# Performance work log

Hardware: AMD Instinct MI355X
Metric: run time of the kernel (lower is better)

## Reference

```python
import jax, jax.numpy as jnp
import numpy as np

N = 100_000      # nodes
E = 1_600_000    # edges (avg degree 16)
D_IN = 128
H = 512


def setup_inputs() -> dict:
    key = jax.random.key(0)
    ks = jax.random.split(key, 7)
    x = jax.random.normal(ks[0], (N, D_IN), dtype=jnp.float32)
    edge_index = jax.random.randint(ks[1], (2, E), 0, N, dtype=jnp.int32)
    s_in = 1.0 / np.sqrt(D_IN).astype(np.float32)
    s_h = 1.0 / np.sqrt(H).astype(np.float32)
    # SAGEConv params: lin_l applied to aggregated neighbors (has bias), lin_r to root
    W_l = jax.random.uniform(ks[2], (D_IN, H), jnp.float32, -s_in, s_in)
    b_l = jax.random.uniform(ks[3], (H,), jnp.float32, -s_in, s_in)
    W_r = jax.random.uniform(ks[4], (D_IN, H), jnp.float32, -s_in, s_in)
    # final projection Linear(hidden, hidden)
    W_proj = jax.random.uniform(ks[5], (H, H), jnp.float32, -s_h, s_h)
    b_proj = jax.random.uniform(ks[6], (H,), jnp.float32, -s_h, s_h)
    return {"x": x, "edge_index": edge_index, "W_l": W_l, "b_l": b_l,
            "W_r": W_r, "W_proj": W_proj, "b_proj": b_proj}


def reference(x, edge_index, W_l, b_l, W_r, W_proj, b_proj):
    src, dst = edge_index[0], edge_index[1]
    # mean aggregation of neighbor features: gather x[src], scatter-add to dst
    agg = jax.ops.segment_sum(x[src], dst, num_segments=N)          # [N, D_IN]
    deg = jax.ops.segment_sum(jnp.ones((E,), x.dtype), dst, num_segments=N)
    mean = agg / jnp.maximum(deg, 1.0)[:, None]
    # SAGEConv: lin_l(mean_neighbors) + lin_r(x)
    h = mean @ W_l + b_l + x @ W_r                                   # [N, H]
    h = jax.nn.relu(h)                                               # dropout: eval mode (identity)
    return h @ W_proj + b_proj                                       # [N, H]
```

## Files before the change

### kernel.cpp

```cpp
#include <hip/hip_runtime.h>
#include <hip/hip_bf16.h>

#define DIN  128
#define HID  512
#define K1   256
#define NPAD 96
#define BSH  8
#define CAPSH 13
#define EPB  4096

typedef __attribute__((ext_vector_type(8))) short short8;
typedef __attribute__((ext_vector_type(4))) float f32x4;

__device__ inline ushort bf16rne(float f) {
    union { float f; unsigned u; } c; c.f = f;
    unsigned b = c.u + 0x7fff + ((c.u >> 16) & 1);
    return (ushort)(b >> 16);
}
__device__ inline float bf16tof(unsigned lo16) {
    union { unsigned u; float f; } c; c.u = lo16 << 16;
    return c.f;
}
__device__ __forceinline__ void gld16(const void* g, void* l) {
    __builtin_amdgcn_global_load_lds((const __attribute__((address_space(1))) unsigned int*)g,
                                     (__attribute__((address_space(3))) unsigned int*)l, 16, 0, 0);
}

__global__ void prep_w(const float* __restrict__ Wl, const float* __restrict__ Wr,
                       const float* __restrict__ Wp,
                       ushort* __restrict__ W1L, ushort* __restrict__ W2L) {
    int t = blockIdx.x * blockDim.x + threadIdx.x;
    if (t < 8 * 4 * 512) {
        int p = t >> 11, c = (t >> 9) & 3, col = t & 511;
        int k0 = p * 32 + c * 8;
        #pragma unroll
        for (int r = 0; r < 8; ++r) {
            int k = k0 + r;
            float v = (k < DIN) ? Wl[k * HID + col] : Wr[(k - DIN) * HID + col];
            W1L[(size_t)t * 8 + r] = bf16rne(v);
        }
    } else if (t < 8 * 4 * 512 + 16 * 4 * 512) {
        int t2 = t - 8 * 4 * 512;
        int p = t2 >> 11, c = (t2 >> 9) & 3, col = t2 & 511;
        int k0 = p * 32 + c * 8;
        #pragma unroll
        for (int r = 0; r < 8; ++r)
            W2L[(size_t)t2 * 8 + r] = bf16rne(Wp[(k0 + r) * HID + col]);
    }
}

__global__ void xcvt(const float* __restrict__ x, ushort* __restrict__ xb, int total4) {
    int i = blockIdx.x * blockDim.x + threadIdx.x;
    if (i >= total4) return;
    const float4 v = ((const float4*)x)[i];
    ushort4 o;
    o.x = bf16rne(v.x); o.y = bf16rne(v.y); o.z = bf16rne(v.z); o.w = bf16rne(v.w);
    ((ushort4*)xb)[i] = o;
}

__global__ void binit_kernel(int* __restrict__ bcur, int nb) {
    int i = threadIdx.x + blockIdx.x * 1024;
    if (i < nb) bcur[i] = i << CAPSH;
}

__global__ __launch_bounds__(256) void bucket_kernel(
    const int* __restrict__ ei, int* __restrict__ bcur,
    unsigned* __restrict__ eb, int E, int nb) {
    __shared__ int lhist[400], lbase[400], lcur[400];
    const int t = threadIdx.x;
    for (int i = t; i < nb; i += 256) lhist[i] = 0;
    __syncthreads();
    const int e0 = blockIdx.x * EPB;
    int srcs[16], dsts[16], bs[16];
    #pragma unroll
    for (int i = 0; i < 16; ++i) {
        int e = e0 + i * 256 + t;
        if (e < E) {
            srcs[i] = ei[e];
            dsts[i] = ei[E + e];
            bs[i] = dsts[i] >> BSH;
            atomicAdd(&lhist[bs[i]], 1);
        } else bs[i] = -1;
    }
    __syncthreads();
    for (int i = t; i < nb; i += 256) {
        lcur[i] = 0;
        if (lhist[i] > 0) lbase[i] = atomicAdd(&bcur[i], lhist[i]);
    }
    __syncthreads();
    #pragma unroll
    for (int i = 0; i < 16; ++i) {
        if (bs[i] >= 0) {
            int off = atomicAdd(&lcur[bs[i]], 1);
            int p = lbase[bs[i]] + off;
            if (p < ((bs[i] + 1) << CAPSH))
                eb[p] = ((unsigned)srcs[i] << 8) | (unsigned)(dsts[i] & 255);
        }
    }
}

__global__ __launch_bounds__(1024) void agg3_kernel(
    const ushort* __restrict__ xb, const unsigned* __restrict__ eb,
    const int* __restrict__ bcur, ushort* __restrict__ mb, int N) {
    __shared__ int sLDS[1 << CAPSH];
    __shared__ int pcnt[256], tmp[256], poff[256], pcur[256];
    const int t = threadIdx.x;
    const int l = t & 63;
    const int wv = t >> 6;
    const int b = blockIdx.x;

    if (t < 256) pcnt[t] = 0;
    __syncthreads();

    const int vbase = b << CAPSH;
    int valid = bcur[b] - vbase;
    if (valid > (1 << CAPSH)) valid = 1 << CAPSH;

    for (int i = t; i < valid; i += 1024)
        atomicAdd(&pcnt[eb[vbase + i] & 255u], 1);
    __syncthreads();

    if (t < 256) tmp[t] = pcnt[t];
    __syncthreads();
    #pragma unroll
    for (int s = 1; s < 256; s <<= 1) {
        int v = 0;
        if (t < 256) { v = tmp[t]; if (t >= s) v += tmp[t - s]; }
        __syncthreads();
        if (t < 256) tmp[t] = v;
        __syncthreads();
    }
    if (t < 256) { poff[t] = tmp[t] - pcnt[t]; pcur[t] = tmp[t] - pcnt[t]; }
    __syncthreads();

    for (int i = t; i < valid; i += 1024) {
        unsigned u = eb[vbase + i];
        int slot = atomicAdd(&pcur[u & 255u], 1);
        sLDS[slot] = (int)(u >> 8);
    }
    __syncthreads();

    for (int nl = wv; nl < 256; nl += 16) {
        int node = (b << BSH) + nl;
        if (node >= N) continue;
        int cn = pcnt[nl];
        const int off = poff[nl];
        float s0 = 0.f, s1 = 0.f;
        int i = 0;
        for (; i + 16 <= cn; i += 16) {
            int s_[16];
            #pragma unroll
            for (int j = 0; j < 16; ++j) s_[j] = sLDS[off + i + j];
            unsigned v_[16];
            #pragma unroll
            for (int j = 0; j < 16; ++j)
                v_[j] = ((const unsigned*)(xb + (size_t)s_[j] * DIN))[l];
            #pragma unroll
            for (int j = 0; j < 16; ++j) {
                s0 += bf16tof(v_[j] & 0xffffu);
                s1 += bf16tof(v_[j] >> 16);
            }
        }
        for (; i + 8 <= cn; i += 8) {
            int s_[8];
            #pragma unroll
            for (int j = 0; j < 8; ++j) s_[j] = sLDS[off + i + j];
            unsigned v_[8];
            #pragma unroll
            for (int j = 0; j < 8; ++j)
                v_[j] = ((const unsigned*)(xb + (size_t)s_[j] * DIN))[l];
            #pragma unroll
            for (int j = 0; j < 8; ++j) {
                s0 += bf16tof(v_[j] & 0xffffu);
                s1 += bf16tof(v_[j] >> 16);
            }
        }
        for (; i + 4 <= cn; i += 4) {
            int s_[4];
            #pragma unroll
            for (int j = 0; j < 4; ++j) s_[j] = sLDS[off + i + j];
            unsigned v_[4];
            #pragma unroll
            for (int j = 0; j < 4; ++j)
                v_[j] = ((const unsigned*)(xb + (size_t)s_[j] * DIN))[l];
            #pragma unroll
            for (int j = 0; j < 4; ++j) {
                s0 += bf16tof(v_[j] & 0xffffu);
                s1 += bf16tof(v_[j] >> 16);
            }
        }
        for (; i < cn; ++i) {
            int src = sLDS[off + i];
            unsigned v = ((const unsigned*)(xb + (size_t)src * DIN))[l];
            s0 += bf16tof(v & 0xffffu);
            s1 += bf16tof(v >> 16);
        }
        float rd = 1.0f / fmaxf((float)cn, 1.0f);
        unsigned o = (unsigned)bf16rne(s0 * rd) | ((unsigned)bf16rne(s1 * rd) << 16);
        ((unsigned*)(mb + (size_t)node * DIN))[l] = o;
    }
}

__global__ void fill_kernel(const int* __restrict__ ei, int* __restrict__ cnt,
                            int* __restrict__ nbr, int E) {
    int e = blockIdx.x * blockDim.x + threadIdx.x;
    if (e >= E) return;
    int src = ei[e];
    int dst = ei[E + e];
    int pos = atomicAdd(cnt + dst, 1);
    if (pos < NPAD) nbr[(size_t)dst * NPAD + pos] = src;
}

__global__ __launch_bounds__(256) void agg_kernel(
    const ushort* __restrict__ xb, const int* __restrict__ cnt, const int* __restrict__ nbr,
    ushort* __restrict__ mb, int N) {
    int node = blockIdx.x * 4 + (threadIdx.x >> 6);
    if (node >= N) return;
    int l = threadIdx.x & 63;
    int cn = cnt[node];
    int cc = cn < NPAD ? cn : NPAD;
    const int* nl = nbr + (size_t)node * NPAD;
    float s0 = 0.f, s1 = 0.f;
    int i = 0;
    for (; i + 4 <= cc; i += 4) {
        int4 q = *(const int4*)(nl + i);
        unsigned v0 = ((const unsigned*)(xb + (size_t)q.x * DIN))[l];
        unsigned v1 = ((const unsigned*)(xb + (size_t)q.y * DIN))[l];
        unsigned v2 = ((const unsigned*)(xb + (size_t)q.z * DIN))[l];
        unsigned v3 = ((const unsigned*)(xb + (size_t)q.w * DIN))[l];
        s0 += bf16tof(v0 & 0xffffu) + bf16tof(v1 & 0xffffu) + bf16tof(v2 & 0xffffu) + bf16tof(v3 & 0xffffu);
        s1 += bf16tof(v0 >> 16) + bf16tof(v1 >> 16) + bf16tof(v2 >> 16) + bf16tof(v3 >> 16);
    }
    for (; i < cc; ++i) {
        int src = nl[i];
        unsigned v = ((const unsigned*)(xb + (size_t)src * DIN))[l];
        s0 += bf16tof(v & 0xffffu);
        s1 += bf16tof(v >> 16);
    }
    float rd = 1.0f / fmaxf((float)cn, 1.0f);
    unsigned o = (unsigned)bf16rne(s0 * rd) | ((unsigned)bf16rne(s1 * rd) << 16);
    ((unsigned*)(mb + (size_t)node * DIN))[l] = o;
}

#define BMT2 128

__global__ __launch_bounds__(1024, 4) void gemm1_kernel(
    const ushort* __restrict__ xb, const ushort* __restrict__ mb,
    const ushort* __restrict__ W1L, const float* __restrict__ bl,
    ushort* __restrict__ Hb, int N) {
    __shared__ unsigned char sm[81920];
    const int t = threadIdx.x;
    const int l = t & 63, w = t >> 6;
    const int wm = w >> 3, wn = w & 7;
    const int lm = l & 15, ch = l >> 4;
    const int base = blockIdx.x * BMT2;

    if (t < 512) {
        int c = t >> 7, row = t & 127;
        int node = base + row; if (node >= N) node = N - 1;
        gld16(mb + (size_t)node * DIN + c * 8, sm + t * 16);
    }
    gld16(W1L + (size_t)t * 8,          sm + 16384 + t * 16);
    gld16(W1L + (size_t)(t + 1024) * 8, sm + 16384 + (t + 1024) * 16);
    __syncthreads();

    f32x4 acc[4][4];
    #pragma unroll
    for (int ct = 0; ct < 4; ++ct) {
        float bv = bl[wn * 64 + ct * 16 + lm];
        #pragma unroll
        for (int f = 0; f < 4; ++f) acc[f][ct] = (f32x4){bv, bv, bv, bv};
    }

    for (int p = 0; p < 8; ++p) {
        if (p < 7) {
            int nb = (p + 1) & 1;
            if (t < 512) {
                int c = t >> 7, row = t & 127;
                int node = base + row; if (node >= N) node = N - 1;
                int k0 = (p + 1) * 32 + c * 8;
                const ushort* src = (k0 < DIN) ? (mb + (size_t)node * DIN + k0)
                                               : (xb + (size_t)node * DIN + (k0 - DIN));
                gld16(src, sm + nb * 8192 + t * 16);
            }
            const ushort* wsrc = W1L + (size_t)(p + 1) * 16384;
            gld16(wsrc + (size_t)t * 8,          sm + 16384 + nb * 32768 + t * 16);
            gld16(wsrc + (size_t)(t + 1024) * 8, sm + 16384 + nb * 32768 + (t + 1024) * 16);
        }
        const unsigned ab = (p & 1) * 8192;
        const unsigned bb = 16384 + (p & 1) * 32768;
        short8 a[4], b[4];
        #pragma unroll
        for (int f = 0; f < 4; ++f)
            a[f] = *(const short8*)(sm + ab + (ch * 128 + wm * 64 + f * 16 + lm) * 16);
        #pragma unroll
        for (int ct = 0; ct < 4; ++ct)
            b[ct] = *(const short8*)(sm + bb + (ch * 512 + wn * 64 + ct * 16 + lm) * 16);
        #pragma unroll
        for (int f = 0; f < 4; ++f)
            #pragma unroll
            for (int ct = 0; ct < 4; ++ct)
                acc[f][ct] = __builtin_amdgcn_mfma_f32_16x16x32_bf16(a[f], b[ct], acc[f][ct], 0, 0, 0);
        __syncthreads();
    }

    #pragma unroll
    for (int f = 0; f < 4; ++f)
        #pragma unroll
        for (int ct = 0; ct < 4; ++ct) {
            int n = wn * 64 + ct * 16 + lm;
            #pragma unroll
            for (int r = 0; r < 4; ++r) {
                int m = wm * 64 + f * 16 + ch * 4 + r;
                int node = base + m;
                if (node < N) Hb[(size_t)node * HID + n] = bf16rne(fmaxf(acc[f][ct][r], 0.0f));
            }
        }
}

__global__ __launch_bounds__(1024, 4) void gemm2_kernel(
    const ushort* __restrict__ Hb, const ushort* __restrict__ W2L,
    const float* __restrict__ bp, float* __restrict__ out, int N) {
    __shared__ unsigned char sm[81920];
    const int t = threadIdx.x;
    const int l = t & 63, w = t >> 6;
    const int wm = w >> 3, wn = w & 7;
    const int lm = l & 15, ch = l >> 4;
    const int base = blockIdx.x * BMT2;

    if (t < 512) {
        int c = t >> 7, row = t & 127;
        int node = base + row; if (node >= N) node = N - 1;
        gld16(Hb + (size_t)node * HID + c * 8, sm + t * 16);
    }
    gld16(W2L + (size_t)t * 8,          sm + 16384 + t * 16);
    gld16(W2L + (size_t)(t + 1024) * 8, sm + 16384 + (t + 1024) * 16);
    __syncthreads();

    f32x4 d[4][4];
    #pragma unroll
    for (int ct = 0; ct < 4; ++ct) {
        float bv = bp[wn * 64 + ct * 16 + lm];
        #pragma unroll
        for (int f = 0; f < 4; ++f) d[f][ct] = (f32x4){bv, bv, bv, bv};
    }

    for (int q = 0; q < 16; ++q) {
        if (q < 15) {
            int nb = (q + 1) & 1;
            if (t < 512) {
                int c = t >> 7, row = t & 127;
                int node = base + row; if (node >= N) node = N - 1;
                gld16(Hb + (size_t)node * HID + (q + 1) * 32 + c * 8, sm + nb * 8192 + t * 16);
            }
            const ushort* wsrc = W2L + (size_t)(q + 1) * 16384;
            gld16(wsrc + (size_t)t * 8,          sm + 16384 + nb * 32768 + t * 16);
            gld16(wsrc + (size_t)(t + 1024) * 8, sm + 16384 + nb * 32768 + (t + 1024) * 16);
        }
        const unsigned ab = (q & 1) * 8192;
        const unsigned bb = 16384 + (q & 1) * 32768;
        short8 a[4], b[4];
        #pragma unroll
        for (int f = 0; f < 4; ++f)
            a[f] = *(const short8*)(sm + ab + (ch * 128 + wm * 64 + f * 16 + lm) * 16);
        #pragma unroll
        for (int ct = 0; ct < 4; ++ct)
            b[ct] = *(const short8*)(sm + bb + (ch * 512 + wn * 64 + ct * 16 + lm) * 16);
        #pragma unroll
        for (int f = 0; f < 4; ++f)
            #pragma unroll
            for (int ct = 0; ct < 4; ++ct)
                d[f][ct] = __builtin_amdgcn_mfma_f32_16x16x32_bf16(a[f], b[ct], d[f][ct], 0, 0, 0);
        __syncthreads();
    }

    #pragma unroll
    for (int f = 0; f < 4; ++f)
        #pragma unroll
        for (int ct = 0; ct < 4; ++ct) {
            int n = wn * 64 + ct * 16 + lm;
            #pragma unroll
            for (int r = 0; r < 4; ++r) {
                int m = wm * 64 + f * 16 + ch * 4 + r;
                int node = base + m;
                if (node < N) out[(size_t)node * HID + n] = d[f][ct][r];
            }
        }
}

#define BMT 64
__global__ __launch_bounds__(1024, 4) void gemm_fused_kernel(
    const ushort* __restrict__ xb, const ushort* __restrict__ mb,
    const ushort* __restrict__ W1L, const ushort* __restrict__ W2L,
    const float* __restrict__ bl, const float* __restrict__ bp,
    float* __restrict__ out, int N) {
    __shared__ unsigned char sm[131072];
    const int t = threadIdx.x;
    const int l = t & 63;
    const int w = t >> 6;
    const int wm = w >> 3;
    const int wn = w & 7;
    const int lm = l & 15;
    const int ch = l >> 4;
    const int base = blockIdx.x * BMT;

    #pragma unroll
    for (int j = 0; j < 2; ++j) {
        int idx = w * 128 + j * 64 + l;
        int p = idx >> 8, c = (idx >> 6) & 3, row = idx & 63;
        int node = base + row;
        if (node >= N) node = N - 1;
        int k0 = p * 32 + c * 8;
        const ushort* src = (k0 < DIN) ? (mb + (size_t)node * DIN + k0)
                                       : (xb + (size_t)node * DIN + (k0 - DIN));
        gld16(src, sm + idx * 16);
    }
    #pragma unroll
    for (int j = 0; j < 2; ++j) {
        int ci = w * 128 + j * 64 + l;
        gld16(W1L + (size_t)ci * 8, sm + 32768 + ci * 16);
    }
    __syncthreads();

    f32x4 acc[2][4];
    #pragma unroll
    for (int ct = 0; ct < 4; ++ct) {
        float bv = bl[wn * 64 + ct * 16 + lm];
        acc[0][ct] = (f32x4){bv, bv, bv, bv};
        acc[1][ct] = acc[0][ct];
    }
    for (int p = 0; p < 8; ++p) {
        if (p < 7) {
            const ushort* wsrc = W1L + (size_t)(p + 1) * 16384;
            unsigned boff = 32768 + (((p + 1) & 1) << 15);
            #pragma unroll
            for (int j = 0; j < 2; ++j) {
                int ci = w * 128 + j * 64 + l;
                gld16(wsrc + (size_t)ci * 8, sm + boff + ci * 16);
            }
        }
        const unsigned abase = (p * 256 + ch * 64) * 16;
        const unsigned bbase = 32768 + ((p & 1) << 15) + ch * 8192;
        short8 a[2], b[4];
        #pragma unroll
        for (int f = 0; f < 2; ++f)
            a[f] = *(const short8*)(sm + abase + (wm * 32 + f * 16 + lm) * 16);
        #pragma unroll
        for (int ct = 0; ct < 4; ++ct)
            b[ct] = *(const short8*)(sm + bbase + (wn * 64 + ct * 16 + lm) * 16);
        #pragma unroll
        for (int f = 0; f < 2; ++f)
            #pragma unroll
            for (int ct = 0; ct < 4; ++ct)
                acc[f][ct] = __builtin_amdgcn_mfma_f32_16x16x32_bf16(a[f], b[ct], acc[f][ct], 0, 0, 0);
        __syncthreads();
    }

    #pragma unroll
    for (int j = 0; j < 2; ++j) {
        int ci = w * 128 + j * 64 + l;
        gld16(W2L + (size_t)ci * 8, sm + 65536 + ci * 16);
    }
    #pragma unroll
    for (int f = 0; f < 2; ++f)
        #pragma unroll
        for (int ct = 0; ct < 4; ++ct) {
            int n = wn * 64 + ct * 16 + lm;
            unsigned hb = ((n >> 5) * 256 + ((n >> 3) & 3) * 64) * 16 + (n & 7) * 2;
            #pragma unroll
            for (int r = 0; r < 4; ++r) {
                int m = wm * 32 + f * 16 + ch * 4 + r;
                *(ushort*)(sm + hb + m * 16) = bf16rne(fmaxf(acc[f][ct][r], 0.0f));
            }
        }
    __syncthreads();

    f32x4 d[2][4];
    #pragma unroll
    for (int ct = 0; ct < 4; ++ct) {
        float bv = bp[wn * 64 + ct * 16 + lm];
        d[0][ct] = (f32x4){bv, bv, bv, bv};
        d[1][ct] = d[0][ct];
    }
    for (int q = 0; q < 16; ++q) {
        if (q < 15) {
            const ushort* wsrc = W2L + (size_t)(q + 1) * 16384;
            unsigned boff = 65536 + (((q + 1) & 1) << 15);
            #pragma unroll
            for (int j = 0; j < 2; ++j) {
                int ci = w * 128 + j * 64 + l;
                gld16(wsrc + (size_t)ci * 8, sm + boff + ci * 16);
            }
        }
        const unsigned abase = (q * 256 + ch * 64) * 16;
        const unsigned bbase = 65536 + ((q & 1) << 15) + ch * 8192;
        short8 a[2], b[4];
        #pragma unroll
        for (int f = 0; f < 2; ++f)
            a[f] = *(const short8*)(sm + abase + (wm * 32 + f * 16 + lm) * 16);
        #pragma unroll
        for (int ct = 0; ct < 4; ++ct)
            b[ct] = *(const short8*)(sm + bbase + (wn * 64 + ct * 16 + lm) * 16);
        #pragma unroll
        for (int f = 0; f < 2; ++f)
            #pragma unroll
            for (int ct = 0; ct < 4; ++ct)
                d[f][ct] = __builtin_amdgcn_mfma_f32_16x16x32_bf16(a[f], b[ct], d[f][ct], 0, 0, 0);
        __syncthreads();
    }

    #pragma unroll
    for (int f = 0; f < 2; ++f)
        #pragma unroll
        for (int ct = 0; ct < 4; ++ct) {
            int n = wn * 64 + ct * 16 + lm;
            #pragma unroll
            for (int r = 0; r < 4; ++r) {
                int m = wm * 32 + f * 16 + ch * 4 + r;
                int node = base + m;
                if (node < N) out[(size_t)node * HID + n] = d[f][ct][r];
            }
        }
}

extern "C" void kernel_launch(void* const* d_in, const int* in_sizes, int n_in,
                              void* d_out, int out_size, void* d_ws, size_t ws_size,
                              hipStream_t stream) {
    const float* x  = (const float*)d_in[0];
    const int*   ei = (const int*)d_in[1];
    const float* Wl = (const float*)d_in[2];
    const float* bl = (const float*)d_in[3];
    const float* Wr = (const float*)d_in[4];
    const float* Wp = (const float*)d_in[5];
    const float* bp = (const float*)d_in[6];
    float* out = (float*)d_out;

    const int N = in_sizes[0] / DIN;
    const int E = in_sizes[1] / 2;
    const int NB = (N + 255) >> BSH;

    const size_t hBytes  = (size_t)N * HID * sizeof(ushort);
    const size_t xbBytes = (size_t)N * DIN * sizeof(ushort);
    const size_t w1Bytes = 131072 * sizeof(ushort);
    const size_t w2Bytes = 262144 * sizeof(ushort);
    const size_t bucketBytes = ((size_t)NB << CAPSH) * sizeof(unsigned) + NB * sizeof(int);
    const size_t needBig = hBytes + 2 * xbBytes + w1Bytes + w2Bytes;

    if (ws_size >= needBig && bucketBytes <= hBytes && N < (1 << 24)) {
        char* base = (char*)d_ws;
        unsigned* eb  = (unsigned*)base;
        int*      bcur = (int*)(eb + ((size_t)NB << CAPSH));
        ushort* Hb   = (ushort*)base;
        ushort* xb   = (ushort*)(base + hBytes);
        ushort* mb   = (ushort*)(base + hBytes + xbBytes);
        ushort* W1L  = (ushort*)(base + hBytes + 2 * xbBytes);
        ushort* W2L  = (ushort*)((char*)W1L + w1Bytes);

        prep_w<<<192, 256, 0, stream>>>(Wl, Wr, Wp, W1L, W2L);
        xcvt<<<((N * DIN / 4) + 255) / 256, 256, 0, stream>>>(x, xb, N * DIN / 4);
        binit_kernel<<<(NB + 1023) / 1024, 1024, 0, stream>>>(bcur, NB);
        bucket_kernel<<<(E + EPB - 1) / EPB, 256, 0, stream>>>(ei, bcur, eb, E, NB);
        agg3_kernel<<<NB, 1024, 0, stream>>>(xb, eb, bcur, mb, N);
        int g = (N + BMT2 - 1) / BMT2;
        gemm1_kernel<<<g, 1024, 0, stream>>>(xb, mb, W1L, bl, Hb, N);
        gemm2_kernel<<<g, 1024, 0, stream>>>(Hb, W2L, bp, out, N);
    } else {
        int*    cnt = (int*)d_ws;
        int*    nbr = cnt + N;
        ushort* xb  = (ushort*)(nbr + (size_t)N * NPAD);
        ushort* mb  = xb + (size_t)N * DIN;
        ushort* W1L = mb + (size_t)N * DIN;
        ushort* W2L = W1L + 131072;

        hipMemsetAsync(cnt, 0, (size_t)N * sizeof(int), stream);
        prep_w<<<192, 256, 0, stream>>>(Wl, Wr, Wp, W1L, W2L);
        xcvt<<<((N * DIN / 4) + 255) / 256, 256, 0, stream>>>(x, xb, N * DIN / 4);
        fill_kernel<<<(E + 255) / 256, 256, 0, stream>>>(ei, cnt, nbr, E);
        agg_kernel<<<(N + 3) / 4, 256, 0, stream>>>(xb, cnt, nbr, mb, N);
        gemm_fused_kernel<<<(N + BMT - 1) / BMT, 1024, 0, stream>>>(xb, mb, W1L, W2L, bl, bp, out, N);
    }
}
```

Before: 275.1 us.

## Merge prep kernels, memset bucket counters, use fine-grained vmcnt waits in GEMMs

```diff
diff --git a/kernel.cpp b/kernel.cpp
--- a/kernel.cpp
+++ b/kernel.cpp
@@ -25,42 +25,43 @@
     __builtin_amdgcn_global_load_lds((const __attribute__((address_space(1))) unsigned int*)g,
                                      (__attribute__((address_space(3))) unsigned int*)l, 16, 0, 0);
 }
-
-__global__ void prep_w(const float* __restrict__ Wl, const float* __restrict__ Wr,
-                       const float* __restrict__ Wp,
-                       ushort* __restrict__ W1L, ushort* __restrict__ W2L) {
-    int t = blockIdx.x * blockDim.x + threadIdx.x;
-    if (t < 8 * 4 * 512) {
-        int p = t >> 11, c = (t >> 9) & 3, col = t & 511;
-        int k0 = p * 32 + c * 8;
-        #pragma unroll
-        for (int r = 0; r < 8; ++r) {
-            int k = k0 + r;
-            float v = (k < DIN) ? Wl[k * HID + col] : Wr[(k - DIN) * HID + col];
-            W1L[(size_t)t * 8 + r] = bf16rne(v);
-        }
-    } else if (t < 8 * 4 * 512 + 16 * 4 * 512) {
-        int t2 = t - 8 * 4 * 512;
-        int p = t2 >> 11, c = (t2 >> 9) & 3, col = t2 & 511;
-        int k0 = p * 32 + c * 8;
-        #pragma unroll
-        for (int r = 0; r < 8; ++r)
-            W2L[(size_t)t2 * 8 + r] = bf16rne(Wp[(k0 + r) * HID + col]);
-    }
-}
-
-__global__ void xcvt(const float* __restrict__ x, ushort* __restrict__ xb, int total4) {
-    int i = blockIdx.x * blockDim.x + threadIdx.x;
-    if (i >= total4) return;
-    const float4 v = ((const float4*)x)[i];
-    ushort4 o;
-    o.x = bf16rne(v.x); o.y = bf16rne(v.y); o.z = bf16rne(v.z); o.w = bf16rne(v.w);
-    ((ushort4*)xb)[i] = o;
-}
-
-__global__ void binit_kernel(int* __restrict__ bcur, int nb) {
-    int i = threadIdx.x + blockIdx.x * 1024;
-    if (i < nb) bcur[i] = i << CAPSH;
+__device__ __forceinline__ void hard_barrier() {
+    __builtin_amdgcn_sched_barrier(0);
+    __builtin_amdgcn_s_barrier();
+    __builtin_amdgcn_sched_barrier(0);
+}
+
+__global__ void prep_all(const float* __restrict__ Wl, const float* __restrict__ Wr,
+                         const float* __restrict__ Wp,
+                         ushort* __restrict__ W1L, ushort* __restrict__ W2L,
+                         const float* __restrict__ x, ushort* __restrict__ xb, int total4) {
+    if (blockIdx.x < 192) {
+        int t = blockIdx.x * 256 + threadIdx.x;
+        if (t < 8 * 4 * 512) {
+            int p = t >> 11, c = (t >> 9) & 3, col = t & 511;
+            int k0 = p * 32 + c * 8;
+            #pragma unroll
+            for (int r = 0; r < 8; ++r) {
+                int k = k0 + r;
+                float v = (k < DIN) ? Wl[k * HID + col] : Wr[(k - DIN) * HID + col];
+                W1L[(size_t)t * 8 + r] = bf16rne(v);
+            }
+        } else {
+            int t2 = t - 8 * 4 * 512;
+            int p = t2 >> 11, c = (t2 >> 9) & 3, col = t2 & 511;
+            int k0 = p * 32 + c * 8;
+            #pragma unroll
+            for (int r = 0; r < 8; ++r)
+                W2L[(size_t)t2 * 8 + r] = bf16rne(Wp[(k0 + r) * HID + col]);
+        }
+    } else {
+        int i = (blockIdx.x - 192) * 256 + threadIdx.x;
+        if (i >= total4) return;
+        const float4 v = ((const float4*)x)[i];
+        ushort4 o;
+        o.x = bf16rne(v.x); o.y = bf16rne(v.y); o.z = bf16rne(v.z); o.w = bf16rne(v.w);
+        ((ushort4*)xb)[i] = o;
+    }
 }
 
 __global__ __launch_bounds__(256) void bucket_kernel(
@@ -92,9 +93,9 @@
     for (int i = 0; i < 16; ++i) {
         if (bs[i] >= 0) {
             int off = atomicAdd(&lcur[bs[i]], 1);
-            int p = lbase[bs[i]] + off;
-            if (p < ((bs[i] + 1) << CAPSH))
-                eb[p] = ((unsigned)srcs[i] << 8) | (unsigned)(dsts[i] & 255);
+            int prel = lbase[bs[i]] + off;
+            if (prel < (1 << CAPSH))
+                eb[((size_t)bs[i] << CAPSH) + prel] = ((unsigned)srcs[i] << 8) | (unsigned)(dsts[i] & 255);
         }
     }
 }
@@ -113,7 +114,7 @@
     __syncthreads();
 
     const int vbase = b << CAPSH;
-    int valid = bcur[b] - vbase;
+    int valid = bcur[b];
     if (valid > (1 << CAPSH)) valid = 1 << CAPSH;
 
     for (int i = t; i < valid; i += 1024)
@@ -262,7 +263,8 @@
     }
     gld16(W1L + (size_t)t * 8,          sm + 16384 + t * 16);
     gld16(W1L + (size_t)(t + 1024) * 8, sm + 16384 + (t + 1024) * 16);
-    __syncthreads();
+    asm volatile("s_waitcnt vmcnt(0)" ::: "memory");
+    hard_barrier();
 
     f32x4 acc[4][4];
     #pragma unroll
@@ -286,7 +288,12 @@
             const ushort* wsrc = W1L + (size_t)(p + 1) * 16384;
             gld16(wsrc + (size_t)t * 8,          sm + 16384 + nb * 32768 + t * 16);
             gld16(wsrc + (size_t)(t + 1024) * 8, sm + 16384 + nb * 32768 + (t + 1024) * 16);
-        }
+            if (t < 512) asm volatile("s_waitcnt vmcnt(3)" ::: "memory");
+            else         asm volatile("s_waitcnt vmcnt(2)" ::: "memory");
+        } else {
+            asm volatile("s_waitcnt vmcnt(0)" ::: "memory");
+        }
+        hard_barrier();
         const unsigned ab = (p & 1) * 8192;
         const unsigned bb = 16384 + (p & 1) * 32768;
         short8 a[4], b[4];
@@ -301,7 +308,7 @@
             #pragma unroll
             for (int ct = 0; ct < 4; ++ct)
                 acc[f][ct] = __builtin_amdgcn_mfma_f32_16x16x32_bf16(a[f], b[ct], acc[f][ct], 0, 0, 0);
-        __syncthreads();
+        hard_barrier();
     }
 
     #pragma unroll
@@ -335,7 +342,8 @@
     }
     gld16(W2L + (size_t)t * 8,          sm + 16384 + t * 16);
     gld16(W2L + (size_t)(t + 1024) * 8, sm + 16384 + (t + 1024) * 16);
-    __syncthreads();
+    asm volatile("s_waitcnt vmcnt(0)" ::: "memory");
+    hard_barrier();
 
     f32x4 d[4][4];
     #pragma unroll
@@ -356,7 +364,12 @@
             const ushort* wsrc = W2L + (size_t)(q + 1) * 16384;
             gld16(wsrc + (size_t)t * 8,          sm + 16384 + nb * 32768 + t * 16);
             gld16(wsrc + (size_t)(t + 1024) * 8, sm + 16384 + nb * 32768 + (t + 1024) * 16);
-        }
+            if (t < 512) asm volatile("s_waitcnt vmcnt(3)" ::: "memory");
+            else         asm volatile("s_waitcnt vmcnt(2)" ::: "memory");
+        } else {
+            asm volatile("s_waitcnt vmcnt(0)" ::: "memory");
+        }
+        hard_barrier();
         const unsigned ab = (q & 1) * 8192;
         const unsigned bb = 16384 + (q & 1) * 32768;
         short8 a[4], b[4];
@@ -371,7 +384,7 @@
             #pragma unroll
             for (int ct = 0; ct < 4; ++ct)
                 d[f][ct] = __builtin_amdgcn_mfma_f32_16x16x32_bf16(a[f], b[ct], d[f][ct], 0, 0, 0);
-        __syncthreads();
+        hard_barrier();
     }
 
     #pragma unroll
@@ -523,6 +536,38 @@
         }
 }
 
+__global__ void prep_w(const float* __restrict__ Wl, const float* __restrict__ Wr,
+                       const float* __restrict__ Wp,
+                       ushort* __restrict__ W1L, ushort* __restrict__ W2L) {
+    int t = blockIdx.x * blockDim.x + threadIdx.x;
+    if (t < 8 * 4 * 512) {
+        int p = t >> 11, c = (t >> 9) & 3, col = t & 511;
+        int k0 = p * 32 + c * 8;
+        #pragma unroll
+        for (int r = 0; r < 8; ++r) {
+            int k = k0 + r;
+            float v = (k < DIN) ? Wl[k * HID + col] : Wr[(k - DIN) * HID + col];
+            W1L[(size_t)t * 8 + r] = bf16rne(v);
+        }
+    } else if (t < 8 * 4 * 512 + 16 * 4 * 512) {
+        int t2 = t - 8 * 4 * 512;
+        int p = t2 >> 11, c = (t2 >> 9) & 3, col = t2 & 511;
+        int k0 = p * 32 + c * 8;
+        #pragma unroll
+        for (int r = 0; r < 8; ++r)
+            W2L[(size_t)t2 * 8 + r] = bf16rne(Wp[(k0 + r) * HID + col]);
+    }
+}
+
+__global__ void xcvt(const float* __restrict__ x, ushort* __restrict__ xb, int total4) {
+    int i = blockIdx.x * blockDim.x + threadIdx.x;
+    if (i >= total4) return;
+    const float4 v = ((const float4*)x)[i];
+    ushort4 o;
+    o.x = bf16rne(v.x); o.y = bf16rne(v.y); o.z = bf16rne(v.z); o.w = bf16rne(v.w);
+    ((ushort4*)xb)[i] = o;
+}
+
 extern "C" void kernel_launch(void* const* d_in, const int* in_sizes, int n_in,
                               void* d_out, int out_size, void* d_ws, size_t ws_size,
                               hipStream_t stream) {
@@ -538,6 +583,7 @@
     const int N = in_sizes[0] / DIN;
     const int E = in_sizes[1] / 2;
     const int NB = (N + 255) >> BSH;
+    const int total4 = N * DIN / 4;
 
     const size_t hBytes  = (size_t)N * HID * sizeof(ushort);
     const size_t xbBytes = (size_t)N * DIN * sizeof(ushort);
@@ -546,7 +592,7 @@
     const size_t bucketBytes = ((size_t)NB << CAPSH) * sizeof(unsigned) + NB * sizeof(int);
     const size_t needBig = hBytes + 2 * xbBytes + w1Bytes + w2Bytes;
 
-    if (ws_size >= needBig && bucketBytes <= hBytes && N < (1 << 24)) {
+    if (ws_size >= needBig && bucketBytes <= hBytes && N < (1 << 24) && NB <= 400) {
         char* base = (char*)d_ws;
         unsigned* eb  = (unsigned*)base;
         int*      bcur = (int*)(eb + ((size_t)NB << CAPSH));
@@ -556,9 +602,8 @@
         ushort* W1L  = (ushort*)(base + hBytes + 2 * xbBytes);
         ushort* W2L  = (ushort*)((char*)W1L + w1Bytes);
 
-        prep_w<<<192, 256, 0, stream>>>(Wl, Wr, Wp, W1L, W2L);
-        xcvt<<<((N * DIN / 4) + 255) / 256, 256, 0, stream>>>(x, xb, N * DIN / 4);
-        binit_kernel<<<(NB + 1023) / 1024, 1024, 0, stream>>>(bcur, NB);
+        hipMemsetAsync(bcur, 0, (size_t)NB * sizeof(int), stream);
+        prep_all<<<192 + (total4 + 255) / 256, 256, 0, stream>>>(Wl, Wr, Wp, W1L, W2L, x, xb, total4);
         bucket_kernel<<<(E + EPB - 1) / EPB, 256, 0, stream>>>(ei, bcur, eb, E, NB);
         agg3_kernel<<<NB, 1024, 0, stream>>>(xb, eb, bcur, mb, N);
         int g = (N + BMT2 - 1) / BMT2;
@@ -574,7 +619,7 @@
 
         hipMemsetAsync(cnt, 0, (size_t)N * sizeof(int), stream);
         prep_w<<<192, 256, 0, stream>>>(Wl, Wr, Wp, W1L, W2L);
-        xcvt<<<((N * DIN / 4) + 255) / 256, 256, 0, stream>>>(x, xb, N * DIN / 4);
+        xcvt<<<(total4 + 255) / 256, 256, 0, stream>>>(x, xb, total4);
         fill_kernel<<<(E + 255) / 256, 256, 0, stream>>>(ei, cnt, nbr, E);
         agg_kernel<<<(N + 3) / 4, 256, 0, stream>>>(xb, cnt, nbr, mb, N);
         gemm_fused_kernel<<<(N + BMT - 1) / BMT, 1024, 0, stream>>>(xb, mb, W1L, W2L, bl, bp, out, N);
```

Measured after the change: 265.1 us, median of 2. -3.6%, faster.
